# Kernel optimization log

Measured on AMD Instinct MI355X. Metric: run time of the kernel, lower is better.

## Reference

```python
import jax, jax.numpy as jnp
import numpy as np

V, D, H, T, B = 32000, 256, 256, 128, 32
SOS = 126


def lstm_cell(x, h, c, Wih, Whh, bih, bhh):
    # torch LSTMCell gate order: i, f, g, o
    z = x @ Wih.T + bih + h @ Whh.T + bhh
    i, f, g, o = jnp.split(z, 4, axis=-1)
    c2 = jax.nn.sigmoid(f) * c + jax.nn.sigmoid(i) * jnp.tanh(g)
    h2 = jax.nn.sigmoid(o) * jnp.tanh(c2)
    return h2, c2


def setup_inputs() -> dict:
    key = jax.random.key(0)
    ks = jax.random.split(key, 22)
    s = 0.05
    rn = lambda k, shp: jax.random.normal(k, shp, jnp.float32) * s
    return {
        'x': jax.random.randint(ks[0], (B, T), 0, V),
        'emb_enc': rn(ks[1], (V, D)),
        'Wih_f': rn(ks[2], (4 * H, D)), 'Whh_f': rn(ks[3], (4 * H, H)),
        'bih_f': rn(ks[4], (4 * H,)), 'bhh_f': rn(ks[5], (4 * H,)),
        'Wih_b': rn(ks[6], (4 * H, D)), 'Whh_b': rn(ks[7], (4 * H, H)),
        'bih_b': rn(ks[8], (4 * H,)), 'bhh_b': rn(ks[9], (4 * H,)),
        'emb_dec': rn(ks[10], (V, D)),
        'Wa_h': rn(ks[11], (2 * H, 2 * H)), 'Wa_e': rn(ks[12], (2 * H, 2 * H)),
        'v_a': rn(ks[13], (2 * H,)), 'b_a': rn(ks[14], (2 * H,)),
        'Wih_d': rn(ks[15], (8 * H, D + 2 * H)), 'Whh_d': rn(ks[16], (8 * H, 2 * H)),
        'bih_d': rn(ks[17], (8 * H,)), 'bhh_d': rn(ks[18], (8 * H,)),
        'Wout': rn(ks[19], (V, 2 * H)), 'bout': rn(ks[20], (V,)),
    }


def reference(x, emb_enc, Wih_f, Whh_f, bih_f, bhh_f, Wih_b, Whh_b, bih_b, bhh_b,
              emb_dec, Wa_h, Wa_e, v_a, b_a, Wih_d, Whh_d, bih_d, bhh_d, Wout, bout):
    # ---- encoder: both directions stepped forward (module feeds one timestep at a time) ----
    h0 = jnp.zeros((B, H), jnp.float32)

    def enc_step(carry, tok):
        hf, cf, hb, cb = carry
        e = emb_enc[tok]                         # (B, D)
        hf, cf = lstm_cell(e, hf, cf, Wih_f, Whh_f, bih_f, bhh_f)
        hb, cb = lstm_cell(e, hb, cb, Wih_b, Whh_b, bih_b, bhh_b)
        return (hf, cf, hb, cb), jnp.concatenate([hf, hb], -1)

    (hf, cf, hb, cb), enc_out = jax.lax.scan(enc_step, (h0, h0, h0, h0), x.T)
    enc_out = enc_out.transpose(1, 0, 2)         # (B, T, 2H)
    proj_e = enc_out @ Wa_e.T                    # precompute attention key proj (B, T, 2H)

    # ---- decoder init: concat bidirectional final states ----
    h = jnp.concatenate([hf, hb], -1)            # (B, 2H)
    c = jnp.concatenate([cf, cb], -1)
    tok0 = jnp.full((B,), SOS, dtype=x.dtype)

    def dec_step(carry, _):
        h, c, tok = carry
        e = emb_dec[tok]                          # (B, D)
        q = h @ Wa_h.T                            # (B, 2H)
        energy = jnp.tanh(proj_e + q[:, None, :] + b_a) @ v_a   # (B, T)
        w = jax.nn.softmax(energy, axis=-1)
        ctx = jnp.einsum('bt,bth->bh', w, enc_out)
        h2, c2 = lstm_cell(jnp.concatenate([e, ctx], -1), h, c, Wih_d, Whh_d, bih_d, bhh_d)
        out = jax.nn.log_softmax(h2 @ Wout.T + bout, axis=-1)    # (B, V)
        nxt = jnp.argmax(out, axis=-1).astype(tok.dtype)
        return (h2, c2, nxt), out

    _, ys = jax.lax.scan(dec_step, (h, c, tok0), None, length=T)  # (T, B, V)
    return ys.transpose(1, 0, 2)                  # (B, T, V)
```

## Files before the change

kernel.cpp:

```cpp
#include <hip/hip_runtime.h>

#define V 32000
#define D 256
#define H 256
#define T 128
#define B 32
#define SOS 126
#define H2 512

#define NBLK 512
#define NTHR 256
#define SCOPE __HIP_MEMORY_SCOPE_AGENT
#define LDS_FLOATS 19456
#define S0 18432

__device__ __forceinline__ float sigf(float x) { return 1.f / (1.f + __expf(-x)); }
__device__ __forceinline__ float ftanh(float x) {
    x = fminf(15.f, fmaxf(-15.f, x));
    float e = __expf(2.f * x);
    return (e - 1.f) / (e + 1.f);
}

__device__ __forceinline__ void gbar(int* __restrict__ slots, int* __restrict__ gen, int tgt) {
    __syncthreads();
    if (blockIdx.x == 0) {
        if (threadIdx.x == 0) {
            __builtin_amdgcn_fence(__ATOMIC_RELEASE, "agent");
            __hip_atomic_store(slots, tgt, __ATOMIC_RELAXED, SCOPE);
        }
        int i0 = (int)threadIdx.x * 2;
        unsigned guard = 0;
        while (__hip_atomic_load(slots + (size_t)i0 * 32, __ATOMIC_RELAXED, SCOPE) < tgt) {
            __builtin_amdgcn_s_sleep(1);
            if (++guard > 100000000u) break;
        }
        guard = 0;
        while (__hip_atomic_load(slots + (size_t)(i0 + 1) * 32, __ATOMIC_RELAXED, SCOPE) < tgt) {
            __builtin_amdgcn_s_sleep(1);
            if (++guard > 100000000u) break;
        }
        __syncthreads();
        if (threadIdx.x == 0) {
            __builtin_amdgcn_fence(__ATOMIC_ACQUIRE, "agent");
            __builtin_amdgcn_fence(__ATOMIC_RELEASE, "agent");
            __hip_atomic_store(gen, tgt, __ATOMIC_RELAXED, SCOPE);
        }
        __syncthreads();
    } else {
        if (threadIdx.x == 0) {
            __builtin_amdgcn_fence(__ATOMIC_RELEASE, "agent");
            __hip_atomic_store(slots + (size_t)blockIdx.x * 32, tgt, __ATOMIC_RELAXED, SCOPE);
            unsigned guard = 0;
            while (__hip_atomic_load(gen, __ATOMIC_RELAXED, SCOPE) < tgt) {
                __builtin_amdgcn_s_sleep(8);
                if (++guard > 100000000u) break;
            }
            __builtin_amdgcn_fence(__ATOMIC_ACQUIRE, "agent");
        }
        __syncthreads();
    }
}

__global__ __launch_bounds__(256) void k_tr(const float* __restrict__ src,
                                            float* __restrict__ dst, int R, int C) {
    __shared__ float tle[32][33];
    int rb = blockIdx.x * 32, cb = blockIdx.y * 32;
    int lr = threadIdx.x & 31, lc = threadIdx.x >> 5;
#pragma unroll
    for (int i = 0; i < 32; i += 8) tle[lc + i][lr] = src[(size_t)(rb + lc + i) * C + cb + lr];
    __syncthreads();
#pragma unroll
    for (int i = 0; i < 32; i += 8) dst[(size_t)(cb + lc + i) * R + rb + lr] = tle[lr][lc + i];
}

__global__ __launch_bounds__(256) void k_prep_encw(
    const float* __restrict__ Wih_f, const float* __restrict__ Whh_f,
    const float* __restrict__ Wih_b, const float* __restrict__ Whh_b,
    float* __restrict__ WencT) {
    int idx = blockIdx.x * 256 + threadIdx.x;
    int k = idx >> 11, col = idx & 2047;
    int dir = col >> 10, cu = col & 1023;
    int u = cu >> 2, g = cu & 3;
    const float* Wih = dir ? Wih_b : Wih_f;
    const float* Whh = dir ? Whh_b : Whh_f;
    float v = (k < 256) ? Wih[(g * H + u) * D + k] : Whh[(g * H + u) * H + (k - 256)];
    WencT[idx] = v;
}

__global__ __launch_bounds__(256) void k_prep_decw(const float* __restrict__ Wih_d,
                                                   const float* __restrict__ Whh_d,
                                                   float* __restrict__ WdT) {
    int idx = blockIdx.x * 256 + threadIdx.x;
    int k = idx >> 11, col = idx & 2047;
    int u = col >> 2, g = col & 3;
    float v = (k < 768) ? Wih_d[(size_t)(g * H2 + u) * 768 + k]
                        : Whh_d[(size_t)(g * H2 + u) * H2 + (k - 768)];
    WdT[idx] = v;
}

__global__ __launch_bounds__(256) void k_norm(float* __restrict__ out,
                                              const float* __restrict__ lse) {
    const int total4 = B * T * V / 4;
    int stride = gridDim.x * 256;
    for (int i4 = blockIdx.x * 256 + threadIdx.x; i4 < total4; i4 += stride) {
        int rowv = i4 / (V / 4);
        float l = lse[rowv];
        float4* p = (float4*)out + i4;
        float4 v = *p;
        v.x -= l; v.y -= l; v.z -= l; v.w -= l;
        *p = v;
    }
}

__global__ __launch_bounds__(256, 2) void k_seq(
    const int* __restrict__ x, const float* __restrict__ emb_enc,
    const float* __restrict__ emb_dec,
    const float* __restrict__ bih_f, const float* __restrict__ bhh_f,
    const float* __restrict__ bih_b, const float* __restrict__ bhh_b,
    const float* __restrict__ bih_d, const float* __restrict__ bhh_d,
    const float* __restrict__ Wa_e, const float* __restrict__ Wa_h,
    const float* __restrict__ b_a, const float* __restrict__ v_a,
    const float* __restrict__ bout,
    const float* __restrict__ WencT, const float* __restrict__ WdT,
    const float* __restrict__ WoutT, const float* __restrict__ WahT,
    float* __restrict__ enc_out, float* __restrict__ proj_e,
    float* __restrict__ cencT, float* __restrict__ zpenc,
    float* __restrict__ hdecT, float* __restrict__ cdecT,
    float* __restrict__ xcatT, float* __restrict__ q_buf, float* __restrict__ zp_h,
    float* __restrict__ Pm, float* __restrict__ Ps,
    int* __restrict__ Pi, float* __restrict__ lse, float* __restrict__ out,
    int* slots, int* gen) {
    extern __shared__ float xs[];
    const int blk = blockIdx.x, tid = threadIdx.x;
    const int kc = (tid >> 3) & 7;
    const int rp = (tid >> 6) * 8 + (tid & 7);
    int bgen = 0;

    for (int t = 0; t <= T; ++t) {
        if (blk < 128) {
            int rowgrp = blk >> 2, c = (blk >> 1) & 1, bh = blk & 1;
            int dir = rowgrp >> 4;
            if (c == 0) {
                if (t < T) {
                    for (int i = tid; i < 4096; i += 256) {
                        int bb = i >> 8, k = i & 255;
                        int tok = x[(bh * 16 + bb) * T + t];
                        xs[k * 20 + bb] = emb_enc[tok * 256 + k];
                    }
                }
            } else {
                if (t == 0) {
                    for (int i = tid; i < 4096; i += 256) {
                        int u = i >> 4, bb = i & 15;
                        xs[u * 20 + bb] = 0.f;
                    }
                } else {
                    bool writer = (rowgrp & 15) == 0;
                    const float* zpp = zpenc + ((t - 1) & 1) * 131072;
                    int pr = t & 1;
                    for (int i = tid; i < 4096; i += 256) {
                        int u = i >> 4, bb = i & 15, bG = bh * 16 + bb;
                        int r = dir * 1024 + u * 4;
                        float z[4];
#pragma unroll
                        for (int g = 0; g < 4; ++g) {
                            float bias = (dir ? bih_b : bih_f)[g * 256 + u] +
                                         (dir ? bhh_b : bhh_f)[g * 256 + u];
                            z[g] = zpp[(size_t)(r + g) * 32 + bG] +
                                   zpp[(size_t)(2048 + r + g) * 32 + bG] + bias;
                        }
                        int ci = ((pr * 2 + dir) * 256 + u) * 32 + bG;
                        float cp = cencT[ci];
                        float c2 = sigf(z[1]) * cp + sigf(z[0]) * ftanh(z[2]);
                        float h2 = sigf(z[3]) * ftanh(c2);
                        xs[u * 20 + bb] = h2;
                        if (writer) {
                            cencT[(((pr ^ 1) * 2 + dir) * 256 + u) * 32 + bG] = c2;
                            enc_out[(size_t)(bG * T + (t - 1)) * H2 + dir * 256 + u] = h2;
                            if (t == T) {
                                hdecT[(dir * 256 + u) * 32 + bG] = h2;
                                cdecT[(dir * 256 + u) * 32 + bG] = c2;
                            }
                        }
                    }
                }
            }
            __syncthreads();
            if (t < T) {
                int r0 = rowgrp * 64 + rp * 2;
                float a0[16], a1[16];
#pragma unroll
                for (int j = 0; j < 16; ++j) { a0[j] = 0.f; a1[j] = 0.f; }
#pragma unroll 4
                for (int j = 0; j < 32; ++j) {
                    int kl = kc + 8 * j;
                    float2 w = *(const float2*)(WencT + (size_t)(c * 256 + kl) * 2048 + r0);
                    const float* xp = xs + kl * 20;
#pragma unroll
                    for (int q = 0; q < 4; ++q) {
                        float4 xv = *(const float4*)(xp + q * 4);
                        a0[q*4+0] = fmaf(w.x, xv.x, a0[q*4+0]); a1[q*4+0] = fmaf(w.y, xv.x, a1[q*4+0]);
                        a0[q*4+1] = fmaf(w.x, xv.y, a0[q*4+1]); a1[q*4+1] = fmaf(w.y, xv.y, a1[q*4+1]);
                        a0[q*4+2] = fmaf(w.x, xv.z, a0[q*4+2]); a1[q*4+2] = fmaf(w.y, xv.z, a1[q*4+2]);
                        a0[q*4+3] = fmaf(w.x, xv.w, a0[q*4+3]); a1[q*4+3] = fmaf(w.y, xv.w, a1[q*4+3]);
                    }
                }
#pragma unroll
                for (int j = 0; j < 16; ++j) {
                    a0[j] += __shfl_xor(a0[j], 8); a0[j] += __shfl_xor(a0[j], 16); a0[j] += __shfl_xor(a0[j], 32);
                    a1[j] += __shfl_xor(a1[j], 8); a1[j] += __shfl_xor(a1[j], 16); a1[j] += __shfl_xor(a1[j], 32);
                }
                if (((tid >> 3) & 7) == 0) {
                    float* zb = zpenc + (t & 1) * 131072 + (size_t)(c * 2048 + r0) * 32 + bh * 16;
#pragma unroll
                    for (int q = 0; q < 4; ++q) {
                        *(float4*)(zb + q * 4)      = make_float4(a0[q*4], a0[q*4+1], a0[q*4+2], a0[q*4+3]);
                        *(float4*)(zb + 32 + q * 4) = make_float4(a1[q*4], a1[q*4+1], a1[q*4+2], a1[q*4+3]);
                    }
                }
            }
        }
        ++bgen; gbar(slots, gen, bgen);
    }

    {
        if (blk < 256) {
            int r0 = blk * 16;
            for (int i = tid; i < 16 * 512; i += 256) {
                int r = i >> 9, k = i & 511;
                xs[r * 512 + k] = enc_out[(size_t)(r0 + r) * H2 + k];
            }
            __syncthreads();
            int j0 = tid * 2;
            float acc0[16], acc1[16];
#pragma unroll
            for (int r = 0; r < 16; ++r) { acc0[r] = 0.f; acc1[r] = 0.f; }
            const float* w0 = Wa_e + j0 * H2;
            const float* w1 = Wa_e + (j0 + 1) * H2;
            for (int k = 0; k < H2; k += 4) {
                float4 wa = *(const float4*)(w0 + k);
                float4 wb = *(const float4*)(w1 + k);
#pragma unroll
                for (int r = 0; r < 16; ++r) {
                    float4 xv = *(const float4*)(&xs[r * 512 + k]);
                    acc0[r] = fmaf(wa.x, xv.x, acc0[r]); acc0[r] = fmaf(wa.y, xv.y, acc0[r]);
                    acc0[r] = fmaf(wa.z, xv.z, acc0[r]); acc0[r] = fmaf(wa.w, xv.w, acc0[r]);
                    acc1[r] = fmaf(wb.x, xv.x, acc1[r]); acc1[r] = fmaf(wb.y, xv.y, acc1[r]);
                    acc1[r] = fmaf(wb.z, xv.z, acc1[r]); acc1[r] = fmaf(wb.w, xv.w, acc1[r]);
                }
            }
#pragma unroll
            for (int r = 0; r < 16; ++r) {
                float2 st; st.x = acc0[r]; st.y = acc1[r];
                *(float2*)(proj_e + (size_t)(r0 + r) * H2 + j0) = st;
            }
        } else if (blk < 320) {
            int gi = (blk - 256) * 256 + tid;
            int j = gi >> 5, b = gi & 31;
            float a0 = 0, a1 = 0, a2 = 0, a3 = 0;
            const float* wr = Wa_h + (size_t)j * H2;
            for (int k = 0; k < H2; k += 4) {
                float4 w = *(const float4*)(wr + k);
                a0 = fmaf(w.x, hdecT[(k    ) * 32 + b], a0);
                a1 = fmaf(w.y, hdecT[(k + 1) * 32 + b], a1);
                a2 = fmaf(w.z, hdecT[(k + 2) * 32 + b], a2);
                a3 = fmaf(w.w, hdecT[(k + 3) * 32 + b], a3);
            }
            q_buf[b * H2 + j] = (a0 + a1) + (a2 + a3);
        }
    }
    ++bgen; gbar(slots, gen, bgen);

    for (int t = 0; t < T; ++t) {
        if (blk < 32) {
            int b = blk;
            int tok = SOS;
            if (t > 0) {
                float* rm = xs + S0; float* rs = rm + 256; int* ri = (int*)(rs + 256);
                float m = -INFINITY, s = 0.f; int mi = 0x7fffffff;
                for (int i = tid; i < 512; i += 256) {
                    if (i < 500) {
                        float m2 = Pm[b * 512 + i], s2 = Ps[b * 512 + i];
                        int i2 = Pi[b * 512 + i];
                        if (m2 > m)      { s = s2 + s * __expf(m - m2); m = m2; mi = i2; }
                        else if (m > m2) { s = s + s2 * __expf(m2 - m); }
                        else             { s = s + s2; mi = (mi < i2) ? mi : i2; }
                    }
                }
                rm[tid] = m; rs[tid] = s; ri[tid] = mi;
                __syncthreads();
                for (int off = 128; off >= 1; off >>= 1) {
                    if (tid < off) {
                        float m1 = rm[tid], m2 = rm[tid + off];
                        float s1 = rs[tid], s2 = rs[tid + off];
                        int i1 = ri[tid], i2 = ri[tid + off];
                        float m_, s_; int i_;
                        if (m2 > m1)      { m_ = m2; s_ = s2 + s1 * __expf(m1 - m2); i_ = i2; }
                        else if (m1 > m2) { m_ = m1; s_ = s1 + s2 * __expf(m2 - m1); i_ = i1; }
                        else              { m_ = m1; s_ = s1 + s2; i_ = (i1 < i2) ? i1 : i2; }
                        rm[tid] = m_; rs[tid] = s_; ri[tid] = i_;
                    }
                    __syncthreads();
                }
                if (tid == 0) lse[b * T + (t - 1)] = rm[0] + logf(rs[0]);
                __syncthreads();
                tok = ri[0];
            }
            xcatT[tid * 32 + b] = emb_dec[tok * 256 + tid];
            float* es = xs + S0;
            {
                int l = tid & 63, w = tid >> 6;
                float4 qb0 = *(const float4*)(q_buf + b * H2 + l * 8);
                float4 qb1 = *(const float4*)(q_buf + b * H2 + l * 8 + 4);
                float4 ba0 = *(const float4*)(b_a + l * 8);
                float4 ba1 = *(const float4*)(b_a + l * 8 + 4);
                qb0.x += ba0.x; qb0.y += ba0.y; qb0.z += ba0.z; qb0.w += ba0.w;
                qb1.x += ba1.x; qb1.y += ba1.y; qb1.z += ba1.z; qb1.w += ba1.w;
                float4 va0 = *(const float4*)(v_a + l * 8);
                float4 va1 = *(const float4*)(v_a + l * 8 + 4);
                for (int tt = w; tt < T; tt += 4) {
                    const float* pp = proj_e + (size_t)(b * T + tt) * H2 + l * 8;
                    float4 p0 = *(const float4*)(pp);
                    float4 p1 = *(const float4*)(pp + 4);
                    float s = ftanh(p0.x + qb0.x) * va0.x + ftanh(p0.y + qb0.y) * va0.y
                            + ftanh(p0.z + qb0.z) * va0.z + ftanh(p0.w + qb0.w) * va0.w
                            + ftanh(p1.x + qb1.x) * va1.x + ftanh(p1.y + qb1.y) * va1.y
                            + ftanh(p1.z + qb1.z) * va1.z + ftanh(p1.w + qb1.w) * va1.w;
#pragma unroll
                    for (int off = 32; off >= 1; off >>= 1) s += __shfl_xor(s, off);
                    if (l == 0) es[tt] = s;
                }
            }
            __syncthreads();
            float* red = xs + S0 + 128; float* wsm = xs + S0 + 256;
            if (tid < 128) red[tid] = es[tid];
            __syncthreads();
            for (int off = 64; off >= 1; off >>= 1) {
                if (tid < off) red[tid] = fmaxf(red[tid], red[tid + off]);
                __syncthreads();
            }
            float M = red[0];
            __syncthreads();
            float ev = 0.f;
            if (tid < 128) { ev = __expf(es[tid] - M); red[tid] = ev; }
            __syncthreads();
            for (int off = 64; off >= 1; off >>= 1) {
                if (tid < off) red[tid] += red[tid + off];
                __syncthreads();
            }
            float S = red[0];
            __syncthreads();
            if (tid < 128) wsm[tid] = ev / S;
            __syncthreads();
            float acc0 = 0.f, acc1 = 0.f;
            const float* eo = enc_out + (size_t)b * T * H2;
#pragma unroll 8
            for (int t2 = 0; t2 < T; ++t2) {
                float wv = wsm[t2];
                acc0 = fmaf(wv, eo[t2 * H2 + tid], acc0);
                acc1 = fmaf(wv, eo[t2 * H2 + tid + 256], acc1);
            }
            xcatT[(256 + tid) * 32 + b] = acc0;
            xcatT[(512 + tid) * 32 + b] = acc1;
        } else if (blk < 288) {
            int m = blk - 32;
            int rl = tid >> 5, b = tid & 31;
            int col = m * 8 + rl;
            float a0 = 0.f, a1 = 0.f;
            const float* wp = WdT + (size_t)768 * 2048 + col;
            const float* xp = hdecT + b;
#pragma unroll 8
            for (int k = 0; k < 512; k += 2) {
                a0 = fmaf(wp[(size_t)k * 2048], xp[k * 32], a0);
                a1 = fmaf(wp[(size_t)(k + 1) * 2048], xp[(k + 1) * 32], a1);
            }
            zp_h[col * 32 + b] = a0 + a1;
        }
        ++bgen; gbar(slots, gen, bgen);

        {
            int u = blk;
            int b = tid & 31, g = (tid >> 5) & 3, kh = tid >> 7;
            int col = u * 4 + g;
            float a0 = 0.f, a1 = 0.f;
            const float* wp = WdT + col;
            const float* xp = xcatT + b;
            int k0 = kh * 384;
#pragma unroll 8
            for (int k = k0; k < k0 + 384; k += 2) {
                a0 = fmaf(wp[(size_t)k * 2048], xp[k * 32], a0);
                a1 = fmaf(wp[(size_t)(k + 1) * 2048], xp[(k + 1) * 32], a1);
            }
            float* zs = xs + S0;
            zs[kh * 128 + g * 32 + b] = a0 + a1;
            __syncthreads();
            if (tid < 32) {
                int bb = tid;
                float z[4];
#pragma unroll
                for (int g2 = 0; g2 < 4; ++g2) {
                    z[g2] = zs[g2 * 32 + bb] + zs[128 + g2 * 32 + bb] +
                            zp_h[(u * 4 + g2) * 32 + bb] +
                            bih_d[g2 * H2 + u] + bhh_d[g2 * H2 + u];
                }
                float cp = cdecT[u * 32 + bb];
                float c2 = sigf(z[1]) * cp + sigf(z[0]) * ftanh(z[2]);
                cdecT[u * 32 + bb] = c2;
                hdecT[u * 32 + bb] = sigf(z[3]) * ftanh(c2);
            }
        }
        ++bgen; gbar(slots, gen, bgen);

        if (blk < 508) {
            for (int i4 = tid; i4 < 4096; i4 += 256) {
                int k = i4 >> 3, b4 = (i4 & 7) * 4;
                *(float4*)(xs + k * 36 + b4) = *(const float4*)(hdecT + k * 32 + b4);
            }
            __syncthreads();
            bool isQ = (blk >= 500);
            const float* wb = isQ ? (WahT + (blk - 500) * 64) : (WoutT + blk * 64);
            const int wst = isQ ? H2 : V;
            int rp2 = rp * 2;
            float a0[32], a1[32];
#pragma unroll
            for (int j = 0; j < 32; ++j) { a0[j] = 0.f; a1[j] = 0.f; }
#pragma unroll 4
            for (int kk = 0; kk < 64; ++kk) {
                int k = kc + 8 * kk;
                float2 w = *(const float2*)(wb + (size_t)k * wst + rp2);
                const float* xp = xs + k * 36;
#pragma unroll
                for (int q = 0; q < 8; ++q) {
                    float4 xv = *(const float4*)(xp + q * 4);
                    a0[q*4+0] = fmaf(w.x, xv.x, a0[q*4+0]); a1[q*4+0] = fmaf(w.y, xv.x, a1[q*4+0]);
                    a0[q*4+1] = fmaf(w.x, xv.y, a0[q*4+1]); a1[q*4+1] = fmaf(w.y, xv.y, a1[q*4+1]);
                    a0[q*4+2] = fmaf(w.x, xv.z, a0[q*4+2]); a1[q*4+2] = fmaf(w.y, xv.z, a1[q*4+2]);
                    a0[q*4+3] = fmaf(w.x, xv.w, a0[q*4+3]); a1[q*4+3] = fmaf(w.y, xv.w, a1[q*4+3]);
                }
            }
#pragma unroll
            for (int j = 0; j < 32; ++j) {
                a0[j] += __shfl_xor(a0[j], 8); a0[j] += __shfl_xor(a0[j], 16); a0[j] += __shfl_xor(a0[j], 32);
                a1[j] += __shfl_xor(a1[j], 8); a1[j] += __shfl_xor(a1[j], 16); a1[j] += __shfl_xor(a1[j], 32);
            }
            __syncthreads();
            if (!isQ) {
                if (((tid >> 3) & 7) == 0) {
#pragma unroll
                    for (int j = 0; j < 32; ++j) {
                        xs[(rp2    ) * 37 + j] = a0[j];
                        xs[(rp2 + 1) * 37 + j] = a1[j];
                    }
                }
                __syncthreads();
                int row0 = blk * 64;
                {
                    int r = tid & 63, bo = tid >> 6;
                    float bv = bout[row0 + r];
#pragma unroll
                    for (int e = 0; e < 8; ++e) {
                        int b = bo * 8 + e;
                        __builtin_nontemporal_store(xs[r * 37 + b] + bv,
                            out + ((size_t)(b * T) + t) * V + row0 + r);
                    }
                }
                float* pm8 = xs + S0; float* ps8 = pm8 + 256; int* pi8 = (int*)(ps8 + 256);
                {
                    int g = tid >> 5, b = tid & 31;
                    float m = -INFINITY, s = 0.f; int mi = 0;
#pragma unroll
                    for (int i = 0; i < 8; ++i) {
                        int rr = g * 8 + i;
                        float v = xs[rr * 37 + b] + bout[row0 + rr];
                        if (v > m) { s *= __expf(m - v); m = v; mi = row0 + rr; }
                        s += __expf(v - m);
                    }
                    pm8[g * 32 + b] = m; ps8[g * 32 + b] = s; pi8[g * 32 + b] = mi;
                }
                __syncthreads();
                if (tid < 32) {
                    int b = tid;
                    float m = pm8[b], s = ps8[b]; int mi = pi8[b];
#pragma unroll
                    for (int g = 1; g < 8; ++g) {
                        float m2 = pm8[g * 32 + b], s2 = ps8[g * 32 + b]; int i2 = pi8[g * 32 + b];
                        if (m2 > m)      { s = s2 + s * __expf(m - m2); m = m2; mi = i2; }
                        else if (m > m2) { s = s + s2 * __expf(m2 - m); }
                        else             { s = s + s2; mi = (mi < i2) ? mi : i2; }
                    }
                    Pm[b * 512 + blk] = m; Ps[b * 512 + blk] = s; Pi[b * 512 + blk] = mi;
                }
            } else {
                if (((tid >> 3) & 7) == 0) {
                    int j0 = (blk - 500) * 64 + rp2;
#pragma unroll
                    for (int b = 0; b < 32; ++b) {
                        q_buf[b * H2 + j0]     = a0[b];
                        q_buf[b * H2 + j0 + 1] = a1[b];
                    }
                }
            }
        }
        ++bgen; gbar(slots, gen, bgen);
    }

    if (blk < 32) {
        int b = blk;
        float* rm = xs + S0; float* rs = rm + 256;
        float m = -INFINITY, s = 0.f;
        for (int i = tid; i < 512; i += 256) {
            if (i < 500) {
                float m2 = Pm[b * 512 + i], s2 = Ps[b * 512 + i];
                if (m2 > m)      { s = s2 + s * __expf(m - m2); m = m2; }
                else if (m > m2) { s = s + s2 * __expf(m2 - m); }
                else             { s = s + s2; }
            }
        }
        rm[tid] = m; rs[tid] = s;
        __syncthreads();
        for (int off = 128; off >= 1; off >>= 1) {
            if (tid < off) {
                float m1 = rm[tid], m2 = rm[tid + off];
                float s1 = rs[tid], s2 = rs[tid + off];
                float m_, s_;
                if (m2 > m1)      { m_ = m2; s_ = s2 + s1 * __expf(m1 - m2); }
                else if (m1 > m2) { m_ = m1; s_ = s1 + s2 * __expf(m2 - m1); }
                else              { m_ = m1; s_ = s1 + s2; }
                rm[tid] = m_; rs[tid] = s_;
            }
            __syncthreads();
        }
        if (tid == 0) lse[b * T + (T - 1)] = rm[0] + logf(rs[0]);
    }
}

extern "C" void kernel_launch(void* const* d_in, const int* in_sizes, int n_in,
                              void* d_out, int out_size, void* d_ws, size_t ws_size,
                              hipStream_t stream) {
    const int* x          = (const int*)d_in[0];
    const float* emb_enc  = (const float*)d_in[1];
    const float* Wih_f    = (const float*)d_in[2];
    const float* Whh_f    = (const float*)d_in[3];
    const float* bih_f    = (const float*)d_in[4];
    const float* bhh_f    = (const float*)d_in[5];
    const float* Wih_b    = (const float*)d_in[6];
    const float* Whh_b    = (const float*)d_in[7];
    const float* bih_b    = (const float*)d_in[8];
    const float* bhh_b    = (const float*)d_in[9];
    const float* emb_dec  = (const float*)d_in[10];
    const float* Wa_h     = (const float*)d_in[11];
    const float* Wa_e     = (const float*)d_in[12];
    const float* v_a      = (const float*)d_in[13];
    const float* b_a      = (const float*)d_in[14];
    const float* Wih_d    = (const float*)d_in[15];
    const float* Whh_d    = (const float*)d_in[16];
    const float* bih_d    = (const float*)d_in[17];
    const float* bhh_d    = (const float*)d_in[18];
    const float* Wout     = (const float*)d_in[19];
    const float* bout     = (const float*)d_in[20];
    float* out = (float*)d_out;

    float* ws = (float*)d_ws;
    size_t o = 0;
    float* enc_out = ws + o; o += (size_t)B * T * H2;
    float* proj_e  = ws + o; o += (size_t)B * T * H2;
    float* WoutT   = ws + o; o += (size_t)H2 * V;
    float* WdT     = ws + o; o += (size_t)1280 * 2048;
    float* WencT   = ws + o; o += (size_t)512 * 2048;
    float* WahT    = ws + o; o += (size_t)H2 * H2;
    float* cencT   = ws + o; o += 2 * 2 * 256 * 32;
    float* zpenc   = ws + o; o += 2 * 2 * 2048 * 32;
    float* hdecT   = ws + o; o += 16384;
    float* cdecT   = ws + o; o += 16384;
    float* xcatT   = ws + o; o += 768 * 32;
    float* q_buf   = ws + o; o += 16384;
    float* zp_h    = ws + o; o += 2048 * 32;
    float* Pm      = ws + o; o += 32 * 512;
    float* Ps      = ws + o; o += 32 * 512;
    float* lse     = ws + o; o += 32 * 128;
    int*   Pi      = (int*)(ws + o); o += 32 * 512;
    int*   slots   = (int*)(ws + o); o += 512 * 32;
    int*   gen     = (int*)(ws + o); o += 32;

    hipMemsetAsync(cencT, 0, 2 * 2 * 256 * 32 * sizeof(float), stream);
    hipMemsetAsync(slots, 0, (512 * 32 + 32) * sizeof(int), stream);

    k_tr<<<dim3(1000, 16), 256, 0, stream>>>(Wout, WoutT, V, H2);
    k_tr<<<dim3(16, 16), 256, 0, stream>>>(Wa_h, WahT, H2, H2);
    k_prep_encw<<<4096, 256, 0, stream>>>(Wih_f, Whh_f, Wih_b, Whh_b, WencT);
    k_prep_decw<<<10240, 256, 0, stream>>>(Wih_d, Whh_d, WdT);

    k_seq<<<NBLK, NTHR, LDS_FLOATS * sizeof(float), stream>>>(
        x, emb_enc, emb_dec,
        bih_f, bhh_f, bih_b, bhh_b, bih_d, bhh_d,
        Wa_e, Wa_h, b_a, v_a, bout,
        WencT, WdT, WoutT, WahT,
        enc_out, proj_e, cencT, zpenc,
        hdecT, cdecT, xcatT, q_buf, zp_h,
        Pm, Ps, Pi, lse, out, slots, gen);

    k_norm<<<4096, 256, 0, stream>>>(out, lse);
}
```

Before: 21.30 ms.

## Lighten grid barriers with relaxed atomics and keep encoder cell state in registers

Replaces the agent-scope release/acquire fences in the grid barrier with relaxed atomic loads and stores on the data that crosses blocks, keeping full fences only at phase boundaries. Encoder cell state moves from a global double-buffered array into per-thread registers. The decoder LSTM matvecs are restructured to stage inputs in LDS and use float4 weight loads, with fewer blocks doing the work. This is meant to cut barrier latency per step, but it relies on every cross-block read and write going through the relaxed atomics to stay correct.

```diff
diff --git a/kernel.cpp b/kernel.cpp
--- a/kernel.cpp
+++ b/kernel.cpp
@@ -21,44 +21,53 @@
     return (e - 1.f) / (e + 1.f);
 }
 
-__device__ __forceinline__ void gbar(int* __restrict__ slots, int* __restrict__ gen, int tgt) {
+__device__ __forceinline__ float lda(const float* p) {
+    return __hip_atomic_load(p, __ATOMIC_RELAXED, SCOPE);
+}
+__device__ __forceinline__ void sta(float* p, float v) {
+    __hip_atomic_store(p, v, __ATOMIC_RELAXED, SCOPE);
+}
+__device__ __forceinline__ int ldai(const int* p) {
+    return __hip_atomic_load(p, __ATOMIC_RELAXED, SCOPE);
+}
+__device__ __forceinline__ void stai(int* p, int v) {
+    __hip_atomic_store(p, v, __ATOMIC_RELAXED, SCOPE);
+}
+
+__device__ __forceinline__ void gbar(int* __restrict__ slots, int* __restrict__ gen,
+                                     int tgt, bool heavy) {
     __syncthreads();
+    if (threadIdx.x == 0) {
+        if (heavy) __builtin_amdgcn_fence(__ATOMIC_RELEASE, "agent");
+        stai(slots + (size_t)blockIdx.x * 32, tgt);
+    }
     if (blockIdx.x == 0) {
-        if (threadIdx.x == 0) {
-            __builtin_amdgcn_fence(__ATOMIC_RELEASE, "agent");
-            __hip_atomic_store(slots, tgt, __ATOMIC_RELAXED, SCOPE);
-        }
         int i0 = (int)threadIdx.x * 2;
-        unsigned guard = 0;
-        while (__hip_atomic_load(slots + (size_t)i0 * 32, __ATOMIC_RELAXED, SCOPE) < tgt) {
+        unsigned g1 = 0;
+        while (ldai(slots + (size_t)i0 * 32) < tgt) {
             __builtin_amdgcn_s_sleep(1);
-            if (++guard > 100000000u) break;
-        }
-        guard = 0;
-        while (__hip_atomic_load(slots + (size_t)(i0 + 1) * 32, __ATOMIC_RELAXED, SCOPE) < tgt) {
+            if (++g1 > 100000000u) break;
+        }
+        g1 = 0;
+        while (ldai(slots + (size_t)(i0 + 1) * 32) < tgt) {
             __builtin_amdgcn_s_sleep(1);
-            if (++guard > 100000000u) break;
-        }
+            if (++g1 > 100000000u) break;
+        }
+        asm volatile("" ::: "memory");
         __syncthreads();
-        if (threadIdx.x == 0) {
-            __builtin_amdgcn_fence(__ATOMIC_ACQUIRE, "agent");
-            __builtin_amdgcn_fence(__ATOMIC_RELEASE, "agent");
-            __hip_atomic_store(gen, tgt, __ATOMIC_RELAXED, SCOPE);
-        }
-        __syncthreads();
+        if (threadIdx.x == 0) stai(gen, tgt);
     } else {
         if (threadIdx.x == 0) {
-            __builtin_amdgcn_fence(__ATOMIC_RELEASE, "agent");
-            __hip_atomic_store(slots + (size_t)blockIdx.x * 32, tgt, __ATOMIC_RELAXED, SCOPE);
-            unsigned guard = 0;
-            while (__hip_atomic_load(gen, __ATOMIC_RELAXED, SCOPE) < tgt) {
-                __builtin_amdgcn_s_sleep(8);
-                if (++guard > 100000000u) break;
-            }
-            __builtin_amdgcn_fence(__ATOMIC_ACQUIRE, "agent");
-        }
-        __syncthreads();
+            unsigned gd = 0;
+            while (ldai(gen) < tgt) {
+                __builtin_amdgcn_s_sleep(4);
+                if (++gd > 100000000u) break;
+            }
+            asm volatile("" ::: "memory");
+        }
     }
+    if (heavy && threadIdx.x == 0) __builtin_amdgcn_fence(__ATOMIC_ACQUIRE, "agent");
+    __syncthreads();
 }
 
 __global__ __launch_bounds__(256) void k_tr(const float* __restrict__ src,
@@ -124,7 +133,7 @@
     const float* __restrict__ WencT, const float* __restrict__ WdT,
     const float* __restrict__ WoutT, const float* __restrict__ WahT,
     float* __restrict__ enc_out, float* __restrict__ proj_e,
-    float* __restrict__ cencT, float* __restrict__ zpenc,
+    float* __restrict__ zpenc,
     float* __restrict__ hdecT, float* __restrict__ cdecT,
     float* __restrict__ xcatT, float* __restrict__ q_buf, float* __restrict__ zp_h,
     float* __restrict__ Pm, float* __restrict__ Ps,
@@ -135,6 +144,7 @@
     const int kc = (tid >> 3) & 7;
     const int rp = (tid >> 6) * 8 + (tid & 7);
     int bgen = 0;
+    float c_priv[16];
 
     for (int t = 0; t <= T; ++t) {
         if (blk < 128) {
@@ -150,15 +160,19 @@
                 }
             } else {
                 if (t == 0) {
-                    for (int i = tid; i < 4096; i += 256) {
+#pragma unroll
+                    for (int j = 0; j < 16; ++j) {
+                        int i = tid + j * 256;
                         int u = i >> 4, bb = i & 15;
                         xs[u * 20 + bb] = 0.f;
+                        c_priv[j] = 0.f;
                     }
                 } else {
                     bool writer = (rowgrp & 15) == 0;
                     const float* zpp = zpenc + ((t - 1) & 1) * 131072;
-                    int pr = t & 1;
-                    for (int i = tid; i < 4096; i += 256) {
+#pragma unroll
+                    for (int j = 0; j < 16; ++j) {
+                        int i = tid + j * 256;
                         int u = i >> 4, bb = i & 15, bG = bh * 16 + bb;
                         int r = dir * 1024 + u * 4;
                         float z[4];
@@ -166,16 +180,15 @@
                         for (int g = 0; g < 4; ++g) {
                             float bias = (dir ? bih_b : bih_f)[g * 256 + u] +
                                          (dir ? bhh_b : bhh_f)[g * 256 + u];
-                            z[g] = zpp[(size_t)(r + g) * 32 + bG] +
-                                   zpp[(size_t)(2048 + r + g) * 32 + bG] + bias;
+                            z[g] = lda(zpp + (size_t)(r + g) * 32 + bG) +
+                                   lda(zpp + (size_t)(2048 + r + g) * 32 + bG) + bias;
                         }
-                        int ci = ((pr * 2 + dir) * 256 + u) * 32 + bG;
-                        float cp = cencT[ci];
+                        float cp = c_priv[j];
                         float c2 = sigf(z[1]) * cp + sigf(z[0]) * ftanh(z[2]);
                         float h2 = sigf(z[3]) * ftanh(c2);
+                        c_priv[j] = c2;
                         xs[u * 20 + bb] = h2;
                         if (writer) {
-                            cencT[(((pr ^ 1) * 2 + dir) * 256 + u) * 32 + bG] = c2;
                             enc_out[(size_t)(bG * T + (t - 1)) * H2 + dir * 256 + u] = h2;
                             if (t == T) {
                                 hdecT[(dir * 256 + u) * 32 + bG] = h2;
@@ -213,14 +226,14 @@
                 if (((tid >> 3) & 7) == 0) {
                     float* zb = zpenc + (t & 1) * 131072 + (size_t)(c * 2048 + r0) * 32 + bh * 16;
 #pragma unroll
-                    for (int q = 0; q < 4; ++q) {
-                        *(float4*)(zb + q * 4)      = make_float4(a0[q*4], a0[q*4+1], a0[q*4+2], a0[q*4+3]);
-                        *(float4*)(zb + 32 + q * 4) = make_float4(a1[q*4], a1[q*4+1], a1[q*4+2], a1[q*4+3]);
-                    }
-                }
-            }
-        }
-        ++bgen; gbar(slots, gen, bgen);
+                    for (int q = 0; q < 16; ++q) {
+                        sta(zb + q, a0[q]);
+                        sta(zb + 32 + q, a1[q]);
+                    }
+                }
+            }
+        }
+        ++bgen; gbar(slots, gen, bgen, t == T);
     }
 
     {
@@ -269,7 +282,7 @@
             q_buf[b * H2 + j] = (a0 + a1) + (a2 + a3);
         }
     }
-    ++bgen; gbar(slots, gen, bgen);
+    ++bgen; gbar(slots, gen, bgen, true);
 
     for (int t = 0; t < T; ++t) {
         if (blk < 32) {
@@ -280,8 +293,8 @@
                 float m = -INFINITY, s = 0.f; int mi = 0x7fffffff;
                 for (int i = tid; i < 512; i += 256) {
                     if (i < 500) {
-                        float m2 = Pm[b * 512 + i], s2 = Ps[b * 512 + i];
-                        int i2 = Pi[b * 512 + i];
+                        float m2 = lda(Pm + b * 512 + i), s2 = lda(Ps + b * 512 + i);
+                        int i2 = ldai(Pi + b * 512 + i);
                         if (m2 > m)      { s = s2 + s * __expf(m - m2); m = m2; mi = i2; }
                         else if (m > m2) { s = s + s2 * __expf(m2 - m); }
                         else             { s = s + s2; mi = (mi < i2) ? mi : i2; }
@@ -306,26 +319,25 @@
                 __syncthreads();
                 tok = ri[0];
             }
-            xcatT[tid * 32 + b] = emb_dec[tok * 256 + tid];
+            sta(xcatT + tid * 32 + b, emb_dec[tok * 256 + tid]);
             float* es = xs + S0;
             {
                 int l = tid & 63, w = tid >> 6;
-                float4 qb0 = *(const float4*)(q_buf + b * H2 + l * 8);
-                float4 qb1 = *(const float4*)(q_buf + b * H2 + l * 8 + 4);
-                float4 ba0 = *(const float4*)(b_a + l * 8);
-                float4 ba1 = *(const float4*)(b_a + l * 8 + 4);
-                qb0.x += ba0.x; qb0.y += ba0.y; qb0.z += ba0.z; qb0.w += ba0.w;
-                qb1.x += ba1.x; qb1.y += ba1.y; qb1.z += ba1.z; qb1.w += ba1.w;
-                float4 va0 = *(const float4*)(v_a + l * 8);
-                float4 va1 = *(const float4*)(v_a + l * 8 + 4);
+                float q8[8], va8[8];
+                const float* qp = q_buf + b * H2 + l * 8;
+#pragma unroll
+                for (int j = 0; j < 8; ++j) {
+                    q8[j] = lda(qp + j) + b_a[l * 8 + j];
+                    va8[j] = v_a[l * 8 + j];
+                }
                 for (int tt = w; tt < T; tt += 4) {
                     const float* pp = proj_e + (size_t)(b * T + tt) * H2 + l * 8;
                     float4 p0 = *(const float4*)(pp);
                     float4 p1 = *(const float4*)(pp + 4);
-                    float s = ftanh(p0.x + qb0.x) * va0.x + ftanh(p0.y + qb0.y) * va0.y
-                            + ftanh(p0.z + qb0.z) * va0.z + ftanh(p0.w + qb0.w) * va0.w
-                            + ftanh(p1.x + qb1.x) * va1.x + ftanh(p1.y + qb1.y) * va1.y
-                            + ftanh(p1.z + qb1.z) * va1.z + ftanh(p1.w + qb1.w) * va1.w;
+                    float s = ftanh(p0.x + q8[0]) * va8[0] + ftanh(p0.y + q8[1]) * va8[1]
+                            + ftanh(p0.z + q8[2]) * va8[2] + ftanh(p0.w + q8[3]) * va8[3]
+                            + ftanh(p1.x + q8[4]) * va8[4] + ftanh(p1.y + q8[5]) * va8[5]
+                            + ftanh(p1.z + q8[6]) * va8[6] + ftanh(p1.w + q8[7]) * va8[7];
 #pragma unroll
                     for (int off = 32; off >= 1; off >>= 1) s += __shfl_xor(s, off);
                     if (l == 0) es[tt] = s;
@@ -360,62 +372,74 @@
                 acc0 = fmaf(wv, eo[t2 * H2 + tid], acc0);
                 acc1 = fmaf(wv, eo[t2 * H2 + tid + 256], acc1);
             }
-            xcatT[(256 + tid) * 32 + b] = acc0;
-            xcatT[(512 + tid) * 32 + b] = acc1;
-        } else if (blk < 288) {
-            int m = blk - 32;
-            int rl = tid >> 5, b = tid & 31;
-            int col = m * 8 + rl;
-            float a0 = 0.f, a1 = 0.f;
-            const float* wp = WdT + (size_t)768 * 2048 + col;
-            const float* xp = hdecT + b;
+            sta(xcatT + (256 + tid) * 32 + b, acc0);
+            sta(xcatT + (512 + tid) * 32 + b, acc1);
+        } else if (blk >= 64 && blk < 128) {
+            int m = blk - 64;
+            for (int i = tid; i < 16384; i += 256) xs[i] = lda(hdecT + i);
+            __syncthreads();
+            int b = tid & 31, cg = tid >> 5;
+            int col0 = m * 32 + cg * 4;
+            float acc[4] = {0.f, 0.f, 0.f, 0.f};
+            const float* wp = WdT + (size_t)768 * 2048 + col0;
 #pragma unroll 8
-            for (int k = 0; k < 512; k += 2) {
-                a0 = fmaf(wp[(size_t)k * 2048], xp[k * 32], a0);
-                a1 = fmaf(wp[(size_t)(k + 1) * 2048], xp[(k + 1) * 32], a1);
-            }
-            zp_h[col * 32 + b] = a0 + a1;
-        }
-        ++bgen; gbar(slots, gen, bgen);
-
-        {
-            int u = blk;
-            int b = tid & 31, g = (tid >> 5) & 3, kh = tid >> 7;
-            int col = u * 4 + g;
-            float a0 = 0.f, a1 = 0.f;
-            const float* wp = WdT + col;
-            const float* xp = xcatT + b;
-            int k0 = kh * 384;
-#pragma unroll 8
-            for (int k = k0; k < k0 + 384; k += 2) {
-                a0 = fmaf(wp[(size_t)k * 2048], xp[k * 32], a0);
-                a1 = fmaf(wp[(size_t)(k + 1) * 2048], xp[(k + 1) * 32], a1);
+            for (int k = 0; k < 512; ++k) {
+                float4 w = *(const float4*)(wp + (size_t)k * 2048);
+                float xv = xs[k * 32 + b];
+                acc[0] = fmaf(w.x, xv, acc[0]); acc[1] = fmaf(w.y, xv, acc[1]);
+                acc[2] = fmaf(w.z, xv, acc[2]); acc[3] = fmaf(w.w, xv, acc[3]);
+            }
+#pragma unroll
+            for (int j = 0; j < 4; ++j) sta(zp_h + (col0 + j) * 32 + b, acc[j]);
+        }
+        ++bgen; gbar(slots, gen, bgen, false);
+
+        if (blk < 128) {
+            int b = tid & 31, cg = (tid >> 5) & 3, kh = tid >> 7;
+            int col0 = blk * 16 + cg * 4;
+            float acc[4] = {0.f, 0.f, 0.f, 0.f};
+            const float* wp = WdT + col0;
+            for (int cc = 0; cc < 2; ++cc) {
+                for (int i = tid; i < 12288; i += 256) xs[i] = lda(xcatT + cc * 12288 + i);
+                __syncthreads();
+                int kbeg = kh * 192;
+#pragma unroll 4
+                for (int kk = 0; kk < 192; ++kk) {
+                    int k = kbeg + kk;
+                    float4 w = *(const float4*)(wp + (size_t)(cc * 384 + k) * 2048);
+                    float xv = xs[k * 32 + b];
+                    acc[0] = fmaf(w.x, xv, acc[0]); acc[1] = fmaf(w.y, xv, acc[1]);
+                    acc[2] = fmaf(w.z, xv, acc[2]); acc[3] = fmaf(w.w, xv, acc[3]);
+                }
+                __syncthreads();
             }
             float* zs = xs + S0;
-            zs[kh * 128 + g * 32 + b] = a0 + a1;
-            __syncthreads();
-            if (tid < 32) {
-                int bb = tid;
+            zs[((kh * 4 + cg) * 4 + 0) * 32 + b] = acc[0];
+            zs[((kh * 4 + cg) * 4 + 1) * 32 + b] = acc[1];
+            zs[((kh * 4 + cg) * 4 + 2) * 32 + b] = acc[2];
+            zs[((kh * 4 + cg) * 4 + 3) * 32 + b] = acc[3];
+            __syncthreads();
+            if (tid < 128) {
+                int ul = tid >> 5, bb = tid & 31;
+                int u = blk * 4 + ul;
                 float z[4];
 #pragma unroll
-                for (int g2 = 0; g2 < 4; ++g2) {
-                    z[g2] = zs[g2 * 32 + bb] + zs[128 + g2 * 32 + bb] +
-                            zp_h[(u * 4 + g2) * 32 + bb] +
-                            bih_d[g2 * H2 + u] + bhh_d[g2 * H2 + u];
-                }
+                for (int g = 0; g < 4; ++g)
+                    z[g] = zs[((0 * 4 + ul) * 4 + g) * 32 + bb]
+                         + zs[((1 * 4 + ul) * 4 + g) * 32 + bb]
+                         + lda(zp_h + (u * 4 + g) * 32 + bb)
+                         + bih_d[g * H2 + u] + bhh_d[g * H2 + u];
                 float cp = cdecT[u * 32 + bb];
-                float c2 = sigf(z[1]) * cp + sigf(z[0]) * ftanh(z[2]);
-                cdecT[u * 32 + bb] = c2;
-                hdecT[u * 32 + bb] = sigf(z[3]) * ftanh(c2);
-            }
-        }
-        ++bgen; gbar(slots, gen, bgen);
+                float c2v = sigf(z[1]) * cp + sigf(z[0]) * ftanh(z[2]);
+                cdecT[u * 32 + bb] = c2v;
+                sta(hdecT + u * 32 + bb, sigf(z[3]) * ftanh(c2v));
+            }
+        }
+        ++bgen; gbar(slots, gen, bgen, false);
 
         if (blk < 508) {
-            for (int i4 = tid; i4 < 4096; i4 += 256) {
-                int k = i4 >> 3, b4 = (i4 & 7) * 4;
-                *(float4*)(xs + k * 36 + b4) = *(const float4*)(hdecT + k * 32 + b4);
-            }
+            for (int i = tid; i < 16384; i += 256)
+                xs[(i >> 5) * 36 + (i & 31)] = lda(hdecT + i);
             __syncthreads();
             bool isQ = (blk >= 500);
             const float* wb = isQ ? (WahT + (blk - 500) * 64) : (WoutT + blk * 64);
@@ -488,20 +512,22 @@
                         else if (m > m2) { s = s + s2 * __expf(m2 - m); }
                         else             { s = s + s2; mi = (mi < i2) ? mi : i2; }
                     }
-                    Pm[b * 512 + blk] = m; Ps[b * 512 + blk] = s; Pi[b * 512 + blk] = mi;
+                    sta(Pm + b * 512 + blk, m);
+                    sta(Ps + b * 512 + blk, s);
+                    stai(Pi + b * 512 + blk, mi);
                 }
             } else {
                 if (((tid >> 3) & 7) == 0) {
                     int j0 = (blk - 500) * 64 + rp2;
 #pragma unroll
                     for (int b = 0; b < 32; ++b) {
-                        q_buf[b * H2 + j0]     = a0[b];
-                        q_buf[b * H2 + j0 + 1] = a1[b];
-                    }
-                }
-            }
-        }
-        ++bgen; gbar(slots, gen, bgen);
+                        sta(q_buf + b * H2 + j0, a0[b]);
+                        sta(q_buf + b * H2 + j0 + 1, a1[b]);
+                    }
+                }
+            }
+        }
+        ++bgen; gbar(slots, gen, bgen, false);
     }
 
     if (blk < 32) {
@@ -510,7 +536,7 @@
         float m = -INFINITY, s = 0.f;
         for (int i = tid; i < 512; i += 256) {
             if (i < 500) {
-                float m2 = Pm[b * 512 + i], s2 = Ps[b * 512 + i];
+                float m2 = lda(Pm + b * 512 + i), s2 = lda(Ps + b * 512 + i);
                 if (m2 > m)      { s = s2 + s * __expf(m - m2); m = m2; }
                 else if (m > m2) { s = s + s2 * __expf(m2 - m); }
                 else             { s = s + s2; }
@@ -568,7 +594,6 @@
     float* WdT     = ws + o; o += (size_t)1280 * 2048;
     float* WencT   = ws + o; o += (size_t)512 * 2048;
     float* WahT    = ws + o; o += (size_t)H2 * H2;
-    float* cencT   = ws + o; o += 2 * 2 * 256 * 32;
     float* zpenc   = ws + o; o += 2 * 2 * 2048 * 32;
     float* hdecT   = ws + o; o += 16384;
     float* cdecT   = ws + o; o += 16384;
@@ -582,7 +607,6 @@
     int*   slots   = (int*)(ws + o); o += 512 * 32;
     int*   gen     = (int*)(ws + o); o += 32;
 
-    hipMemsetAsync(cencT, 0, 2 * 2 * 256 * 32 * sizeof(float), stream);
     hipMemsetAsync(slots, 0, (512 * 32 + 32) * sizeof(int), stream);
 
     k_tr<<<dim3(1000, 16), 256, 0, stream>>>(Wout, WoutT, V, H2);
@@ -595,7 +619,7 @@
         bih_f, bhh_f, bih_b, bhh_b, bih_d, bhh_d,
         Wa_e, Wa_h, b_a, v_a, bout,
         WencT, WdT, WoutT, WahT,
-        enc_out, proj_e, cencT, zpenc,
+        enc_out, proj_e, zpenc,
         hdecT, cdecT, xcatT, q_buf, zp_h,
         Pm, Ps, Pi, lse, out, slots, gen);
 
```

Result: slower. 50.24 ms (+135.9%).
